# Kernel optimization log

Measured on AMD Instinct MI355X. Metric: run time of the kernel, lower is better.

The kernel has to match this reference:

```python
import jax, jax.numpy as jnp
import numpy as np

B = 262144
N = 256      # mode size of every TT core
R = 8        # tt_rank
D = 8        # number of cores = 7 state dims + 1 action dim
STD = 0.001


def setup_inputs() -> dict:
    key = jax.random.key(0)
    ks = jax.random.split(key, D + 2)
    inp = {}
    # TT cores: G0 (1,N,R), G1..G6 (R,N,R), G7 (R,N,1)
    inp["G0"] = jax.random.normal(ks[0], (1, N, R), dtype=jnp.float32) * STD
    for k in range(1, D - 1):
        inp[f"G{k}"] = jax.random.normal(ks[k], (R, N, R), dtype=jnp.float32) * STD
    inp[f"G{D-1}"] = jax.random.normal(ks[D - 1], (R, N, 1), dtype=jnp.float32) * STD
    inp["states"] = jax.random.randint(ks[D], (B, 7), 0, N, dtype=jnp.int32)
    inp["actions"] = jax.random.randint(ks[D + 1], (B,), 0, N, dtype=jnp.int32)
    return inp


def reference(G0, G1, G2, G3, G4, G5, G6, G7, states, actions):
    # mode 'q_sa': concat state indices with action index -> (B, D)
    idx = jnp.concatenate(
        [states.reshape(-1, 7), actions.reshape(-1, 1)], axis=1
    )
    cores = [G0, G1, G2, G3, G4, G5, G6, G7]
    # t3f.gather_nd: chain of per-core gathers + tiny batched matmuls.
    # vec starts as the gathered slice of the first core: (B, R)
    vec = cores[0][0, idx[:, 0], :]
    for k in range(1, D):
        # gather slices along mode axis: (B, r_prev, r_next)
        sl = jnp.transpose(jnp.take(cores[k], idx[:, k], axis=1), (1, 0, 2))
        vec = jnp.einsum("br,brs->bs", vec, sl)
    # final vec has shape (B, 1); Q(s,a) values per batch element
    return vec[:, 0]
```

## Files before the change

### kernel.cpp

```cpp
#include <hip/hip_runtime.h>


#define NN 256
#define RR 8
#define NR 2048
#define U67_OFF 524288
#define GT_OFF  1048576
#define GT_CORE 16384

__device__ __forceinline__ unsigned short f2bf_rne(float f) {
    unsigned int u = __float_as_uint(f);
    u += 0x7FFFu + ((u >> 16) & 1u);
    return (unsigned short)(u >> 16);
}

__device__ __forceinline__ uint4 pack8bf(const float* a) {
    return make_uint4(
        f2bf_rne(a[0]) | ((unsigned int)f2bf_rne(a[1]) << 16),
        f2bf_rne(a[2]) | ((unsigned int)f2bf_rne(a[3]) << 16),
        f2bf_rne(a[4]) | ((unsigned int)f2bf_rne(a[5]) << 16),
        f2bf_rne(a[6]) | ((unsigned int)f2bf_rne(a[7]) << 16));
}

__global__ __launch_bounds__(256) void build_tables(
    const float* __restrict__ G0, const float* __restrict__ G1,
    const float* __restrict__ G2, const float* __restrict__ G3,
    const float* __restrict__ G4, const float* __restrict__ G5,
    const float* __restrict__ G6, const float* __restrict__ G7,
    unsigned short* __restrict__ wsb) {
    const int t = threadIdx.x;
    const int bid = blockIdx.x;

    if (bid < NN) {
        const int n0 = bid, n1 = t;
        float acc[RR] = {0.f,0.f,0.f,0.f,0.f,0.f,0.f,0.f};
#pragma unroll
        for (int r = 0; r < RR; ++r) {
            float ar = G0[n0 * RR + r];
            const float4* p = (const float4*)(G1 + r * NR + n1 * RR);
            float4 x = p[0], y = p[1];
            acc[0] += ar * x.x; acc[1] += ar * x.y;
            acc[2] += ar * x.z; acc[3] += ar * x.w;
            acc[4] += ar * y.x; acc[5] += ar * y.y;
            acc[6] += ar * y.z; acc[7] += ar * y.w;
        }
        *(uint4*)(wsb + n0 * 2048 + n1 * 8) = pack8bf(acc);
    } else if (bid < 2 * NN) {
        const int n6 = bid - NN, n7 = t;
        float g7v[RR];
#pragma unroll
        for (int s = 0; s < RR; ++s) g7v[s] = G7[s * NN + n7];
        float u[RR];
#pragma unroll
        for (int r = 0; r < RR; ++r) {
            float acc = 0.f;
#pragma unroll
            for (int s = 0; s < RR; ++s)
                acc += G6[r * NR + n6 * RR + s] * g7v[s];
            u[r] = acc;
        }
        *(uint4*)(wsb + U67_OFF + n6 * 2048 + n7 * 8) = pack8bf(u);
    } else {
        const int q = bid - 2 * NN;
        const int k = q >> 3;
        const int chunk = q & 7;
        const float* __restrict__ Gk =
            (k == 0) ? G2 : (k == 1) ? G3 : (k == 2) ? G4 : G5;
        const int n = chunk * 32 + (t >> 3);
        const int r = t & 7;
        const float4* src = (const float4*)(Gk + r * NR + n * RR);
        float4 x = src[0], y = src[1];
        float a[8] = {x.x, x.y, x.z, x.w, y.x, y.y, y.z, y.w};
        *(uint4*)(wsb + GT_OFF + k * GT_CORE + r * 2048 + n * 8) = pack8bf(a);
    }
}

#define BF2F_LO(u) __uint_as_float((u) << 16)
#define BF2F_HI(u) __uint_as_float((u) & 0xFFFF0000u)

#define LP(q0, q1, k, nk, rp)                                               \
    do {                                                                    \
        const uint4* _p = l4 + (k) * 2048 + (nk) + (rp) * 512;              \
        q0 = _p[0];                                                         \
        q1 = _p[256];                                                       \
    } while (0)

#define FP(q0, q1, rp)                                                      \
    do {                                                                    \
        const float wa = v[2 * (rp)], wb = v[2 * (rp) + 1];                 \
        acc[0] += wa * BF2F_LO(q0.x); acc[0] += wb * BF2F_LO(q1.x);         \
        acc[1] += wa * BF2F_HI(q0.x); acc[1] += wb * BF2F_HI(q1.x);         \
        acc[2] += wa * BF2F_LO(q0.y); acc[2] += wb * BF2F_LO(q1.y);         \
        acc[3] += wa * BF2F_HI(q0.y); acc[3] += wb * BF2F_HI(q1.y);         \
        acc[4] += wa * BF2F_LO(q0.z); acc[4] += wb * BF2F_LO(q1.z);         \
        acc[5] += wa * BF2F_HI(q0.z); acc[5] += wb * BF2F_HI(q1.z);         \
        acc[6] += wa * BF2F_LO(q0.w); acc[6] += wb * BF2F_LO(q1.w);         \
        acc[7] += wa * BF2F_HI(q0.w); acc[7] += wb * BF2F_HI(q1.w);         \
    } while (0)

#define ENDST                                                               \
    do {                                                                    \
        _Pragma("unroll") for (int i = 0; i < 8; ++i) {                     \
            v[i] = acc[i]; acc[i] = 0.f;                                    \
        }                                                                   \
    } while (0)

__global__ __launch_bounds__(512, 2) void tt_gather(
    const unsigned short* __restrict__ wsb,
    const int* __restrict__ states, const int* __restrict__ actions,
    float* __restrict__ out, int B) {
    __shared__ unsigned short lut[4 * GT_CORE];

    const int t = threadIdx.x;
    const int b = blockIdx.x * 512 + t;
    const bool active = (b < B);
    const int base = active ? b * 7 : 0;
    const int s0 = states[base + 0] & 255;
    const int s1 = states[base + 1] & 255;
    const int s2 = states[base + 2] & 255;
    const int s3 = states[base + 3] & 255;
    const int s4 = states[base + 4] & 255;
    const int s5 = states[base + 5] & 255;
    const int s6 = states[base + 6] & 255;
    const int a7 = actions[active ? b : 0] & 255;

    const uint4 uv = *(const uint4*)(wsb + s0 * 2048 + s1 * 8);
    const uint4 ue = *(const uint4*)(wsb + U67_OFF + s6 * 2048 + a7 * 8);

    {
        const uint4* src = (const uint4*)(wsb + GT_OFF);
        uint4* dst = (uint4*)lut;
#pragma unroll
        for (int i = 0; i < 16; ++i) dst[t + (i << 9)] = src[t + (i << 9)];
    }
    __syncthreads();

    float v[8], acc[8];
    v[0] = BF2F_LO(uv.x); v[1] = BF2F_HI(uv.x);
    v[2] = BF2F_LO(uv.y); v[3] = BF2F_HI(uv.y);
    v[4] = BF2F_LO(uv.z); v[5] = BF2F_HI(uv.z);
    v[6] = BF2F_LO(uv.w); v[7] = BF2F_HI(uv.w);
#pragma unroll
    for (int i = 0; i < 8; ++i) acc[i] = 0.f;

    const uint4* l4 = (const uint4*)lut;
    uint4 X0, X1, Y0, Y1, Z0, Z1;

    LP(X0, X1, 0, s2, 0);
    LP(Y0, Y1, 0, s2, 1);
    LP(Z0, Z1, 0, s2, 2);  FP(X0, X1, 0);
    LP(X0, X1, 0, s2, 3);  FP(Y0, Y1, 1);
    LP(Y0, Y1, 1, s3, 0);  FP(Z0, Z1, 2);
    LP(Z0, Z1, 1, s3, 1);  FP(X0, X1, 3);  ENDST;
    LP(X0, X1, 1, s3, 2);  FP(Y0, Y1, 0);
    LP(Y0, Y1, 1, s3, 3);  FP(Z0, Z1, 1);
    LP(Z0, Z1, 2, s4, 0);  FP(X0, X1, 2);
    LP(X0, X1, 2, s4, 1);  FP(Y0, Y1, 3);  ENDST;
    LP(Y0, Y1, 2, s4, 2);  FP(Z0, Z1, 0);
    LP(Z0, Z1, 2, s4, 3);  FP(X0, X1, 1);
    LP(X0, X1, 3, s5, 0);  FP(Y0, Y1, 2);
    LP(Y0, Y1, 3, s5, 1);  FP(Z0, Z1, 3);  ENDST;
    LP(Z0, Z1, 3, s5, 2);  FP(X0, X1, 0);
    LP(X0, X1, 3, s5, 3);  FP(Y0, Y1, 1);
                           FP(Z0, Z1, 2);
                           FP(X0, X1, 3);  ENDST;

    float q = v[0] * BF2F_LO(ue.x) + v[1] * BF2F_HI(ue.x)
            + v[2] * BF2F_LO(ue.y) + v[3] * BF2F_HI(ue.y)
            + v[4] * BF2F_LO(ue.z) + v[5] * BF2F_HI(ue.z)
            + v[6] * BF2F_LO(ue.w) + v[7] * BF2F_HI(ue.w);
    if (active) out[b] = q;
}

extern "C" void kernel_launch(void* const* d_in, const int* in_sizes, int n_in,
                              void* d_out, int out_size, void* d_ws, size_t ws_size,
                              hipStream_t stream) {
    const float* G0 = (const float*)d_in[0];
    const float* G1 = (const float*)d_in[1];
    const float* G2 = (const float*)d_in[2];
    const float* G3 = (const float*)d_in[3];
    const float* G4 = (const float*)d_in[4];
    const float* G5 = (const float*)d_in[5];
    const float* G6 = (const float*)d_in[6];
    const float* G7 = (const float*)d_in[7];
    const int* states  = (const int*)d_in[8];
    const int* actions = (const int*)d_in[9];
    float* out = (float*)d_out;
    int B = in_sizes[9];

    unsigned short* wsb = (unsigned short*)d_ws;

    hipLaunchKernelGGL(build_tables, dim3(2 * NN + 32), dim3(256), 0, stream,
                       G0, G1, G2, G3, G4, G5, G6, G7, wsb);

    hipLaunchKernelGGL(tt_gather, dim3((B + 511) / 512), dim3(512), 0, stream,
                       wsb, states, actions, out, B);
}
```

Baseline: 89.99 us.

## Fuse table build into gather kernel with double-buffered per-core LDS staging

Drops the separate precompute kernel that built the G0·G1 and G6·G7 pair tables and the transposed bf16 middle cores. Each block now converts each core (G1..G6) from fp32 to bf16 itself and stages it into a double-buffered shared-memory region, overlapping the staging of the next core with the chain step on the current one. The last step reads G7 from shared memory in fp32. This removes one kernel launch and the large pair-table gathers from global memory. In exchange there are two more chain steps, five extra block-wide barriers, and every block repeats the conversion of all cores from global memory.

```diff
diff --git a/kernel.cpp b/kernel.cpp
--- a/kernel.cpp
+++ b/kernel.cpp
@@ -4,9 +4,6 @@
 #define NN 256
 #define RR 8
 #define NR 2048
-#define U67_OFF 524288
-#define GT_OFF  1048576
-#define GT_CORE 16384
 
 __device__ __forceinline__ unsigned short f2bf_rne(float f) {
     unsigned int u = __float_as_uint(f);
@@ -22,70 +19,22 @@
         f2bf_rne(a[6]) | ((unsigned int)f2bf_rne(a[7]) << 16));
 }
 
-__global__ __launch_bounds__(256) void build_tables(
-    const float* __restrict__ G0, const float* __restrict__ G1,
-    const float* __restrict__ G2, const float* __restrict__ G3,
-    const float* __restrict__ G4, const float* __restrict__ G5,
-    const float* __restrict__ G6, const float* __restrict__ G7,
-    unsigned short* __restrict__ wsb) {
-    const int t = threadIdx.x;
-    const int bid = blockIdx.x;
-
-    if (bid < NN) {
-        const int n0 = bid, n1 = t;
-        float acc[RR] = {0.f,0.f,0.f,0.f,0.f,0.f,0.f,0.f};
-#pragma unroll
-        for (int r = 0; r < RR; ++r) {
-            float ar = G0[n0 * RR + r];
-            const float4* p = (const float4*)(G1 + r * NR + n1 * RR);
-            float4 x = p[0], y = p[1];
-            acc[0] += ar * x.x; acc[1] += ar * x.y;
-            acc[2] += ar * x.z; acc[3] += ar * x.w;
-            acc[4] += ar * y.x; acc[5] += ar * y.y;
-            acc[6] += ar * y.z; acc[7] += ar * y.w;
-        }
-        *(uint4*)(wsb + n0 * 2048 + n1 * 8) = pack8bf(acc);
-    } else if (bid < 2 * NN) {
-        const int n6 = bid - NN, n7 = t;
-        float g7v[RR];
-#pragma unroll
-        for (int s = 0; s < RR; ++s) g7v[s] = G7[s * NN + n7];
-        float u[RR];
-#pragma unroll
-        for (int r = 0; r < RR; ++r) {
-            float acc = 0.f;
-#pragma unroll
-            for (int s = 0; s < RR; ++s)
-                acc += G6[r * NR + n6 * RR + s] * g7v[s];
-            u[r] = acc;
-        }
-        *(uint4*)(wsb + U67_OFF + n6 * 2048 + n7 * 8) = pack8bf(u);
-    } else {
-        const int q = bid - 2 * NN;
-        const int k = q >> 3;
-        const int chunk = q & 7;
-        const float* __restrict__ Gk =
-            (k == 0) ? G2 : (k == 1) ? G3 : (k == 2) ? G4 : G5;
-        const int n = chunk * 32 + (t >> 3);
-        const int r = t & 7;
-        const float4* src = (const float4*)(Gk + r * NR + n * RR);
-        float4 x = src[0], y = src[1];
-        float a[8] = {x.x, x.y, x.z, x.w, y.x, y.y, y.z, y.w};
-        *(uint4*)(wsb + GT_OFF + k * GT_CORE + r * 2048 + n * 8) = pack8bf(a);
-    }
-}
-
 #define BF2F_LO(u) __uint_as_float((u) << 16)
 #define BF2F_HI(u) __uint_as_float((u) & 0xFFFF0000u)
 
-#define LP(q0, q1, k, nk, rp)                                               \
+#define STAGE_NEXT(nc, Gsrc)                                                \
     do {                                                                    \
-        const uint4* _p = l4 + (k) * 2048 + (nk) + (rp) * 512;              \
-        q0 = _p[0];                                                         \
-        q1 = _p[256];                                                       \
+        _Pragma("unroll") for (int i = 0; i < 4; ++i) {                     \
+            const int p = (i << 9) + t;                        \
+            const int r = p >> 8, n = p & 255;                              \
+            const float4* sp = (const float4*)((Gsrc) + r * NR + n * RR);   \
+            float4 x = sp[0], y = sp[1];                                    \
+            float a8[8] = {x.x, x.y, x.z, x.w, y.x, y.y, y.z, y.w};         \
+            lbuf[(nc) * 2048 + r * 256 + n] = pack8bf(a8);                  \
+        }                                                                   \
     } while (0)
 
-#define FP(q0, q1, rp)                                                      \
+#define FPX(q0, q1, rp)                                                     \
     do {                                                                    \
         const float wa = v[2 * (rp)], wb = v[2 * (rp) + 1];                 \
         acc[0] += wa * BF2F_LO(q0.x); acc[0] += wb * BF2F_LO(q1.x);         \
@@ -98,19 +47,32 @@
         acc[7] += wa * BF2F_HI(q0.w); acc[7] += wb * BF2F_HI(q1.w);         \
     } while (0)
 
-#define ENDST                                                               \
+#define PHASE_CHAIN(c, nidx)                                                \
     do {                                                                    \
-        _Pragma("unroll") for (int i = 0; i < 8; ++i) {                     \
-            v[i] = acc[i]; acc[i] = 0.f;                                    \
-        }                                                                   \
+        const uint4* mp = lbuf + (c) * 2048 + (nidx);                       \
+        uint4 P0 = mp[0],   P1 = mp[256];                                   \
+        uint4 Q0 = mp[512], Q1 = mp[768];                                   \
+        float acc[8] = {0.f,0.f,0.f,0.f,0.f,0.f,0.f,0.f};                   \
+        FPX(P0, P1, 0);                                                     \
+        P0 = mp[1024]; P1 = mp[1280];                                       \
+        FPX(Q0, Q1, 1);                                                     \
+        Q0 = mp[1536]; Q1 = mp[1792];                                       \
+        FPX(P0, P1, 2);                                                     \
+        FPX(Q0, Q1, 3);                                                     \
+        _Pragma("unroll") for (int i = 0; i < 8; ++i) v[i] = acc[i];        \
     } while (0)
 
-__global__ __launch_bounds__(512, 2) void tt_gather(
-    const unsigned short* __restrict__ wsb,
+__global__ __launch_bounds__(512, 2) void tt_fused(
+    const float* __restrict__ G0, const float* __restrict__ G1,
+    const float* __restrict__ G2, const float* __restrict__ G3,
+    const float* __restrict__ G4, const float* __restrict__ G5,
+    const float* __restrict__ G6, const float* __restrict__ G7,
     const int* __restrict__ states, const int* __restrict__ actions,
     float* __restrict__ out, int B) {
-    __shared__ unsigned short lut[4 * GT_CORE];
+    __shared__ unsigned short lut[2 * 16384];
+    __shared__ float g7s[2048];
 
+    uint4* lbuf = (uint4*)lut;
     const int t = threadIdx.x;
     const int b = blockIdx.x * 512 + t;
     const bool active = (b < B);
@@ -124,51 +86,26 @@
     const int s6 = states[base + 6] & 255;
     const int a7 = actions[active ? b : 0] & 255;
 
-    const uint4 uv = *(const uint4*)(wsb + s0 * 2048 + s1 * 8);
-    const uint4 ue = *(const uint4*)(wsb + U67_OFF + s6 * 2048 + a7 * 8);
+    const float4* g0p = (const float4*)(G0 + s0 * RR);
+    const float4 v0a = g0p[0], v0b = g0p[1];
 
-    {
-        const uint4* src = (const uint4*)(wsb + GT_OFF);
-        uint4* dst = (uint4*)lut;
-#pragma unroll
-        for (int i = 0; i < 16; ++i) dst[t + (i << 9)] = src[t + (i << 9)];
-    }
+    ((float4*)g7s)[t] = ((const float4*)G7)[t];
+    STAGE_NEXT(0, G1);
     __syncthreads();
 
-    float v[8], acc[8];
-    v[0] = BF2F_LO(uv.x); v[1] = BF2F_HI(uv.x);
-    v[2] = BF2F_LO(uv.y); v[3] = BF2F_HI(uv.y);
-    v[4] = BF2F_LO(uv.z); v[5] = BF2F_HI(uv.z);
-    v[6] = BF2F_LO(uv.w); v[7] = BF2F_HI(uv.w);
+    float v[8] = {v0a.x, v0a.y, v0a.z, v0a.w, v0b.x, v0b.y, v0b.z, v0b.w};
+
+    STAGE_NEXT(1, G2);  PHASE_CHAIN(0, s1);  __syncthreads();
+    STAGE_NEXT(0, G3);  PHASE_CHAIN(1, s2);  __syncthreads();
+    STAGE_NEXT(1, G4);  PHASE_CHAIN(0, s3);  __syncthreads();
+    STAGE_NEXT(0, G5);  PHASE_CHAIN(1, s4);  __syncthreads();
+    STAGE_NEXT(1, G6);  PHASE_CHAIN(0, s5);  __syncthreads();
+                        PHASE_CHAIN(1, s6);
+
+    float q = 0.f;
 #pragma unroll
-    for (int i = 0; i < 8; ++i) acc[i] = 0.f;
+    for (int r = 0; r < RR; ++r) q += v[r] * g7s[r * NN + a7];
 
-    const uint4* l4 = (const uint4*)lut;
-    uint4 X0, X1, Y0, Y1, Z0, Z1;
-
-    LP(X0, X1, 0, s2, 0);
-    LP(Y0, Y1, 0, s2, 1);
-    LP(Z0, Z1, 0, s2, 2);  FP(X0, X1, 0);
-    LP(X0, X1, 0, s2, 3);  FP(Y0, Y1, 1);
-    LP(Y0, Y1, 1, s3, 0);  FP(Z0, Z1, 2);
-    LP(Z0, Z1, 1, s3, 1);  FP(X0, X1, 3);  ENDST;
-    LP(X0, X1, 1, s3, 2);  FP(Y0, Y1, 0);
-    LP(Y0, Y1, 1, s3, 3);  FP(Z0, Z1, 1);
-    LP(Z0, Z1, 2, s4, 0);  FP(X0, X1, 2);
-    LP(X0, X1, 2, s4, 1);  FP(Y0, Y1, 3);  ENDST;
-    LP(Y0, Y1, 2, s4, 2);  FP(Z0, Z1, 0);
-    LP(Z0, Z1, 2, s4, 3);  FP(X0, X1, 1);
-    LP(X0, X1, 3, s5, 0);  FP(Y0, Y1, 2);
-    LP(Y0, Y1, 3, s5, 1);  FP(Z0, Z1, 3);  ENDST;
-    LP(Z0, Z1, 3, s5, 2);  FP(X0, X1, 0);
-    LP(X0, X1, 3, s5, 3);  FP(Y0, Y1, 1);
-                           FP(Z0, Z1, 2);
-                           FP(X0, X1, 3);  ENDST;
-
-    float q = v[0] * BF2F_LO(ue.x) + v[1] * BF2F_HI(ue.x)
-            + v[2] * BF2F_LO(ue.y) + v[3] * BF2F_HI(ue.y)
-            + v[4] * BF2F_LO(ue.z) + v[5] * BF2F_HI(ue.z)
-            + v[6] * BF2F_LO(ue.w) + v[7] * BF2F_HI(ue.w);
     if (active) out[b] = q;
 }
 
@@ -188,11 +125,9 @@
     float* out = (float*)d_out;
     int B = in_sizes[9];
 
-    unsigned short* wsb = (unsigned short*)d_ws;
+    (void)d_ws; (void)ws_size;
 
-    hipLaunchKernelGGL(build_tables, dim3(2 * NN + 32), dim3(256), 0, stream,
-                       G0, G1, G2, G3, G4, G5, G6, G7, wsb);
-
-    hipLaunchKernelGGL(tt_gather, dim3((B + 511) / 512), dim3(512), 0, stream,
-                       wsb, states, actions, out, B);
+    hipLaunchKernelGGL(tt_fused, dim3((B + 511) / 512), dim3(512), 0, stream,
+                       G0, G1, G2, G3, G4, G5, G6, G7,
+                       states, actions, out, B);
 }
```

After: 95.00 us. +5.6%, slower.

## Split gather chain into two kernels with half-size LDS tables

Applied to the files above, without the earlier changes.

Splits the single gather kernel into two passes: one contracts cores 2-3 and writes an 8-float intermediate per batch element to workspace, the second contracts cores 4-5 and finishes with the precomputed G6·G7 table. Each pass stages only two cores into LDS (64 KB instead of 128 KB) and converts fp32 cores to bf16 in-kernel, so the separate transpose step in the table builder is dropped. The aim is higher occupancy per CU. The cost is an extra launch, 8 MB of intermediate global traffic, and re-reading the states array in both passes.

```diff
diff --git a/kernel.cpp b/kernel.cpp
--- a/kernel.cpp
+++ b/kernel.cpp
@@ -5,8 +5,7 @@
 #define RR 8
 #define NR 2048
 #define U67_OFF 524288
-#define GT_OFF  1048576
-#define GT_CORE 16384
+#define VT_OFF  1048576
 
 __device__ __forceinline__ unsigned short f2bf_rne(float f) {
     unsigned int u = __float_as_uint(f);
@@ -24,8 +23,6 @@
 
 __global__ __launch_bounds__(256) void build_tables(
     const float* __restrict__ G0, const float* __restrict__ G1,
-    const float* __restrict__ G2, const float* __restrict__ G3,
-    const float* __restrict__ G4, const float* __restrict__ G5,
     const float* __restrict__ G6, const float* __restrict__ G7,
     unsigned short* __restrict__ wsb) {
     const int t = threadIdx.x;
@@ -45,7 +42,7 @@
             acc[6] += ar * y.z; acc[7] += ar * y.w;
         }
         *(uint4*)(wsb + n0 * 2048 + n1 * 8) = pack8bf(acc);
-    } else if (bid < 2 * NN) {
+    } else {
         const int n6 = bid - NN, n7 = t;
         float g7v[RR];
 #pragma unroll
@@ -60,27 +57,27 @@
             u[r] = acc;
         }
         *(uint4*)(wsb + U67_OFF + n6 * 2048 + n7 * 8) = pack8bf(u);
-    } else {
-        const int q = bid - 2 * NN;
-        const int k = q >> 3;
-        const int chunk = q & 7;
-        const float* __restrict__ Gk =
-            (k == 0) ? G2 : (k == 1) ? G3 : (k == 2) ? G4 : G5;
-        const int n = chunk * 32 + (t >> 3);
-        const int r = t & 7;
-        const float4* src = (const float4*)(Gk + r * NR + n * RR);
-        float4 x = src[0], y = src[1];
-        float a[8] = {x.x, x.y, x.z, x.w, y.x, y.y, y.z, y.w};
-        *(uint4*)(wsb + GT_OFF + k * GT_CORE + r * 2048 + n * 8) = pack8bf(a);
     }
 }
 
 #define BF2F_LO(u) __uint_as_float((u) << 16)
 #define BF2F_HI(u) __uint_as_float((u) & 0xFFFF0000u)
 
-#define LP(q0, q1, k, nk, rp)                                               \
-    do {                                                                    \
-        const uint4* _p = l4 + (k) * 2048 + (nk) + (rp) * 512;              \
+#define STAGE_CORE(kc, Gk)                                                  \
+    do {                                                                    \
+        _Pragma("unroll") for (int i = 0; i < 4; ++i) {                     \
+            const int p = (i << 9) + t;                        \
+            const int r = p >> 8, n = p & 255;                              \
+            const float4* sp = (const float4*)((Gk) + r * NR + n * RR);     \
+            float4 x = sp[0], y = sp[1];                                    \
+            float a8[8] = {x.x, x.y, x.z, x.w, y.x, y.y, y.z, y.w};         \
+            ((uint4*)lut)[(kc) * 2048 + r * 256 + n] = pack8bf(a8);         \
+        }                                                                   \
+    } while (0)
+
+#define LP(q0, q1, kc, nk, rp)                                              \
+    do {                                                                    \
+        const uint4* _p = l4 + (kc) * 2048 + (nk) + (rp) * 512;             \
         q0 = _p[0];                                                         \
         q1 = _p[256];                                                       \
     } while (0)
@@ -105,11 +102,26 @@
         }                                                                   \
     } while (0)
 
-__global__ __launch_bounds__(512, 2) void tt_gather(
+#define CHAIN2(c0, c1)                                                      \
+    do {                                                                    \
+        uint4 X0, X1, Y0, Y1, Z0, Z1;                                       \
+        LP(X0, X1, 0, c0, 0);                                               \
+        LP(Y0, Y1, 0, c0, 1);                                               \
+        LP(Z0, Z1, 0, c0, 2);  FP(X0, X1, 0);                               \
+        LP(X0, X1, 0, c0, 3);  FP(Y0, Y1, 1);                               \
+        LP(Y0, Y1, 1, c1, 0);  FP(Z0, Z1, 2);                               \
+        LP(Z0, Z1, 1, c1, 1);  FP(X0, X1, 3);  ENDST;                       \
+        LP(X0, X1, 1, c1, 2);  FP(Y0, Y1, 0);                               \
+        LP(Y0, Y1, 1, c1, 3);  FP(Z0, Z1, 1);                               \
+                               FP(X0, X1, 2);                               \
+                               FP(Y0, Y1, 3);  ENDST;                       \
+    } while (0)
+
+__global__ __launch_bounds__(512, 2) void tt_lo(
     const unsigned short* __restrict__ wsb,
-    const int* __restrict__ states, const int* __restrict__ actions,
-    float* __restrict__ out, int B) {
-    __shared__ unsigned short lut[4 * GT_CORE];
+    const float* __restrict__ G2, const float* __restrict__ G3,
+    const int* __restrict__ states, float* __restrict__ vtmp, int B) {
+    __shared__ unsigned short lut[2 * 16384];
 
     const int t = threadIdx.x;
     const int b = blockIdx.x * 512 + t;
@@ -119,20 +131,11 @@
     const int s1 = states[base + 1] & 255;
     const int s2 = states[base + 2] & 255;
     const int s3 = states[base + 3] & 255;
-    const int s4 = states[base + 4] & 255;
-    const int s5 = states[base + 5] & 255;
-    const int s6 = states[base + 6] & 255;
-    const int a7 = actions[active ? b : 0] & 255;
 
     const uint4 uv = *(const uint4*)(wsb + s0 * 2048 + s1 * 8);
-    const uint4 ue = *(const uint4*)(wsb + U67_OFF + s6 * 2048 + a7 * 8);
-
-    {
-        const uint4* src = (const uint4*)(wsb + GT_OFF);
-        uint4* dst = (uint4*)lut;
-#pragma unroll
-        for (int i = 0; i < 16; ++i) dst[t + (i << 9)] = src[t + (i << 9)];
-    }
+
+    STAGE_CORE(0, G2);
+    STAGE_CORE(1, G3);
     __syncthreads();
 
     float v[8], acc[8];
@@ -144,26 +147,47 @@
     for (int i = 0; i < 8; ++i) acc[i] = 0.f;
 
     const uint4* l4 = (const uint4*)lut;
-    uint4 X0, X1, Y0, Y1, Z0, Z1;
-
-    LP(X0, X1, 0, s2, 0);
-    LP(Y0, Y1, 0, s2, 1);
-    LP(Z0, Z1, 0, s2, 2);  FP(X0, X1, 0);
-    LP(X0, X1, 0, s2, 3);  FP(Y0, Y1, 1);
-    LP(Y0, Y1, 1, s3, 0);  FP(Z0, Z1, 2);
-    LP(Z0, Z1, 1, s3, 1);  FP(X0, X1, 3);  ENDST;
-    LP(X0, X1, 1, s3, 2);  FP(Y0, Y1, 0);
-    LP(Y0, Y1, 1, s3, 3);  FP(Z0, Z1, 1);
-    LP(Z0, Z1, 2, s4, 0);  FP(X0, X1, 2);
-    LP(X0, X1, 2, s4, 1);  FP(Y0, Y1, 3);  ENDST;
-    LP(Y0, Y1, 2, s4, 2);  FP(Z0, Z1, 0);
-    LP(Z0, Z1, 2, s4, 3);  FP(X0, X1, 1);
-    LP(X0, X1, 3, s5, 0);  FP(Y0, Y1, 2);
-    LP(Y0, Y1, 3, s5, 1);  FP(Z0, Z1, 3);  ENDST;
-    LP(Z0, Z1, 3, s5, 2);  FP(X0, X1, 0);
-    LP(X0, X1, 3, s5, 3);  FP(Y0, Y1, 1);
-                           FP(Z0, Z1, 2);
-                           FP(X0, X1, 3);  ENDST;
+    CHAIN2(s2, s3);
+
+    if (active) {
+        float4* vo = (float4*)(vtmp + b * 8);
+        vo[0] = make_float4(v[0], v[1], v[2], v[3]);
+        vo[1] = make_float4(v[4], v[5], v[6], v[7]);
+    }
+}
+
+__global__ __launch_bounds__(512, 2) void tt_hi(
+    const unsigned short* __restrict__ wsb,
+    const float* __restrict__ G4, const float* __restrict__ G5,
+    const int* __restrict__ states, const int* __restrict__ actions,
+    const float* __restrict__ vtmp, float* __restrict__ out, int B) {
+    __shared__ unsigned short lut[2 * 16384];
+
+    const int t = threadIdx.x;
+    const int b = blockIdx.x * 512 + t;
+    const bool active = (b < B);
+    const int base = active ? b * 7 : 0;
+    const int s4 = states[base + 4] & 255;
+    const int s5 = states[base + 5] & 255;
+    const int s6 = states[base + 6] & 255;
+    const int a7 = actions[active ? b : 0] & 255;
+
+    const float4* vi = (const float4*)(vtmp + (active ? b : 0) * 8);
+    const float4 va = vi[0], vb = vi[1];
+    const uint4 ue = *(const uint4*)(wsb + U67_OFF + s6 * 2048 + a7 * 8);
+
+    STAGE_CORE(0, G4);
+    STAGE_CORE(1, G5);
+    __syncthreads();
+
+    float v[8], acc[8];
+    v[0] = va.x; v[1] = va.y; v[2] = va.z; v[3] = va.w;
+    v[4] = vb.x; v[5] = vb.y; v[6] = vb.z; v[7] = vb.w;
+#pragma unroll
+    for (int i = 0; i < 8; ++i) acc[i] = 0.f;
+
+    const uint4* l4 = (const uint4*)lut;
+    CHAIN2(s4, s5);
 
     float q = v[0] * BF2F_LO(ue.x) + v[1] * BF2F_HI(ue.x)
             + v[2] * BF2F_LO(ue.y) + v[3] * BF2F_HI(ue.y)
@@ -189,10 +213,14 @@
     int B = in_sizes[9];
 
     unsigned short* wsb = (unsigned short*)d_ws;
-
-    hipLaunchKernelGGL(build_tables, dim3(2 * NN + 32), dim3(256), 0, stream,
-                       G0, G1, G2, G3, G4, G5, G6, G7, wsb);
-
-    hipLaunchKernelGGL(tt_gather, dim3((B + 511) / 512), dim3(512), 0, stream,
-                       wsb, states, actions, out, B);
-}
+    float* vtmp = (float*)(wsb + VT_OFF);
+
+    const int nblk = (B + 511) / 512;
+
+    hipLaunchKernelGGL(build_tables, dim3(2 * NN), dim3(256), 0, stream,
+                       G0, G1, G6, G7, wsb);
+    hipLaunchKernelGGL(tt_lo, dim3(nblk), dim3(512), 0, stream,
+                       wsb, G2, G3, states, vtmp, B);
+    hipLaunchKernelGGL(tt_hi, dim3(nblk), dim3(512), 0, stream,
+                       wsb, G4, G5, states, actions, vtmp, out, B);
+}
```

Measured after the change: 95.38 us. +6.0%, slower.
